# Performance work log

Hardware: AMD Instinct MI355X
Metric: run time of the kernel (lower is better)

The kernel has to match this reference:

```python
import jax, jax.numpy as jnp
import numpy as np

N_NODES = 100001      # total_nodes + 1
N_EDGES = 6400000     # avg degree ~64
LATENT_DIM = 32
N_LAYERS = 2


def setup_inputs() -> dict:
    key = jax.random.key(0)
    k1, k2, k3, k4 = jax.random.split(key, 4)
    emb_weight = jax.random.normal(k1, (N_NODES, LATENT_DIM), dtype=jnp.float32) * 0.1
    adj_vals = jax.random.uniform(k2, (N_EDGES,), dtype=jnp.float32)
    adj_row = jax.random.randint(k3, (N_EDGES,), 0, N_NODES, dtype=jnp.int32)
    adj_col = jax.random.randint(k4, (N_EDGES,), 0, N_NODES, dtype=jnp.int32)
    return {"emb_weight": emb_weight, "adj_vals": adj_vals,
            "adj_row": adj_row, "adj_col": adj_col}


def reference(emb_weight, adj_vals, adj_row, adj_col):
    n = emb_weight.shape[0]

    def spmm(x):
        # y[r] = sum_{e: row[e]==r} vals[e] * x[col[e]]  (torch.sparse.mm COO)
        gathered = adj_vals[:, None] * x[adj_col]  # [E, D]
        return jax.ops.segment_sum(gathered, adj_row, num_segments=n)

    emb = emb_weight
    acc = emb                      # layer-0 embedding
    for _ in range(N_LAYERS):
        emb = spmm(emb)
        acc = acc + emb
    # mean over (n_layers + 1) stacked embeddings
    return acc / jnp.float32(N_LAYERS + 1)
```

## Files before the change

kernel.cpp:

```cpp
#include <hip/hip_runtime.h>


constexpr int D = 32;
constexpr int RPB_LOG = 8;
constexpr int RPB = 1 << RPB_LOG;
constexpr int MAXNB = 512;
constexpr int TILE = 4096;
constexpr int PT2 = 512;
constexpr int CAP = 9728;
constexpr float QSCALE = 32768.0f;
constexpr float QINV = 1.0f / 32768.0f;

__device__ __forceinline__ unsigned short f2bf(float f) {
    unsigned u = __float_as_uint(f);
    unsigned r = (u + 0x7FFFu + ((u >> 16) & 1u)) >> 16;
    return (unsigned short)r;
}
__device__ __forceinline__ float bf2f(unsigned short h) {
    return __uint_as_float((unsigned)h << 16);
}

__global__ void zero_f32(float* __restrict__ p, int n) {
    int i = blockIdx.x * blockDim.x + threadIdx.x;
    if (i < n) p[i] = 0.0f;
}
__global__ void cast_bf16(const float* __restrict__ in,
                          unsigned short* __restrict__ out, int n) {
    int i = blockIdx.x * blockDim.x + threadIdx.x;
    if (i < n) out[i] = f2bf(in[i]);
}

__global__ __launch_bounds__(256) void tile_hist(
    const int* __restrict__ row, int* __restrict__ tileCnt, int nE, int NB) {
    __shared__ int h[MAXNB];
    int tile = blockIdx.x;
    int base = tile * TILE;
    int n = min(TILE, nE - base);
    int t = threadIdx.x;
    for (int i = t; i < NB; i += 256) h[i] = 0;
    __syncthreads();
    for (int i = t; i < n; i += 256)
        atomicAdd(&h[row[base + i] >> RPB_LOG], 1);
    __syncthreads();
    for (int i = t; i < NB; i += 256)
        tileCnt[(size_t)tile * NB + i] = h[i];
}

__global__ __launch_bounds__(256) void colscan(
    int* __restrict__ tileCnt, int* __restrict__ cnt, int nTiles, int NB) {
    __shared__ int s2[256];
    __shared__ int carryS;
    int b = blockIdx.x, t = threadIdx.x;
    if (t == 0) carryS = 0;
    __syncthreads();
    for (int c0 = 0; c0 < nTiles; c0 += 1024) {
        int v[4], idx[4];
        int sum = 0;
#pragma unroll
        for (int k = 0; k < 4; ++k) {
            idx[k] = c0 + t * 4 + k;
            v[k] = (idx[k] < nTiles) ? tileCnt[(size_t)idx[k] * NB + b] : 0;
            sum += v[k];
        }
        s2[t] = sum;
        __syncthreads();
        for (int o = 1; o < 256; o <<= 1) {
            int x = (t >= o) ? s2[t - o] : 0;
            __syncthreads();
            s2[t] += x;
            __syncthreads();
        }
        int run = ((t == 0) ? 0 : s2[t - 1]) + carryS;
#pragma unroll
        for (int k = 0; k < 4; ++k) {
            if (idx[k] < nTiles) tileCnt[(size_t)idx[k] * NB + b] = run;
            run += v[k];
        }
        __syncthreads();
        if (t == 0) carryS += s2[255];
        __syncthreads();
    }
    if (t == 0) cnt[b] = carryS;
}

__global__ __launch_bounds__(512) void scan_buckets(
    const int* __restrict__ cnt, int* __restrict__ bases, int NB, int nE) {
    __shared__ int s[MAXNB];
    int t = threadIdx.x;
    s[t] = (t < NB) ? cnt[t] : 0;
    __syncthreads();
    for (int o = 1; o < 512; o <<= 1) {
        int v = (t >= o) ? s[t - o] : 0;
        __syncthreads();
        s[t] += v;
        __syncthreads();
    }
    if (t < NB) bases[t] = (t == 0) ? 0 : s[t - 1];
    if (t == 0) bases[NB] = nE;
}

__global__ __launch_bounds__(PT2) void partition_edges2(
    const int* __restrict__ row, const int* __restrict__ col,
    const float* __restrict__ vals, const int* __restrict__ bases,
    const int* __restrict__ tileCnt, uint2* __restrict__ cv, int nE, int NB) {
    __shared__ uint2 buf[TILE];
    __shared__ unsigned short bkt[TILE];
    __shared__ int hist[MAXNB];
    __shared__ int runoff[MAXNB];
    __shared__ int s2[PT2];
    int t = threadIdx.x;
    int tile = blockIdx.x;
    int base = tile * TILE;
    int n = min(TILE, nE - base);
    if (n <= 0) return;
    for (int i = t; i < NB; i += PT2) hist[i] = 0;
    __syncthreads();
    for (int i = t; i < n; i += PT2)
        atomicAdd(&hist[row[base + i] >> RPB_LOG], 1);
    __syncthreads();
    {
        int a0 = (t < NB) ? hist[t] : 0;
        s2[t] = a0;
        __syncthreads();
        for (int o = 1; o < PT2; o <<= 1) {
            int v = (t >= o) ? s2[t - o] : 0;
            __syncthreads();
            s2[t] += v;
            __syncthreads();
        }
        if (t < NB) runoff[t] = s2[t] - a0;
    }
    __syncthreads();
    for (int i = t; i < NB; i += PT2)
        hist[i] = bases[i] + tileCnt[(size_t)tile * NB + i] - runoff[i];
    __syncthreads();
    for (int i = t; i < n; i += PT2) {
        int r = row[base + i];
        int b = r >> RPB_LOG;
        int slot = atomicAdd(&runoff[b], 1);
        float v = vals[base + i];
        int q = __float2int_rn(v * QSCALE);
        q = max(0, min(32767, q));
        uint2 p;
        p.x = (unsigned)col[base + i] | ((unsigned)(r & (RPB - 1)) << 17);
        p.y = (unsigned)q;
        buf[slot] = p;
        bkt[slot] = (unsigned short)b;
    }
    __syncthreads();
    for (int i = t; i < n; i += PT2)
        cv[hist[bkt[i]] + i] = buf[i];
}

__global__ __launch_bounds__(512) void csr_sort4(
    const int* __restrict__ bases, const uint2* __restrict__ cv,
    unsigned* __restrict__ cv2, int* __restrict__ rowptr, int n, int nE) {
    __shared__ unsigned stage[CAP];
    __shared__ int hist_s[RPB];
    __shared__ int cur_s[RPB];
    int t = threadIdx.x;
    int b = blockIdx.x >> 1;
    int h = blockIdx.x & 1;
    int s = bases[b], e = bases[b + 1];
    if (t < RPB) hist_s[t] = 0;
    __syncthreads();
    for (int i = s + t; i < e; i += 512)
        atomicAdd(&hist_s[cv[i].x >> 17], 1);
    __syncthreads();
    if (t < RPB) cur_s[t] = hist_s[t];
    __syncthreads();
    for (int o = 1; o < RPB; o <<= 1) {
        int v = 0;
        if (t < RPB && t >= o) v = cur_s[t - o];
        __syncthreads();
        if (t < RPB) cur_s[t] += v;
        __syncthreads();
    }
    int excl = 0;
    if (t < RPB) excl = (t == 0) ? 0 : cur_s[t - 1];
    int half_lo = h << 7;
    __syncthreads();
    int base_h = (half_lo == 0) ? 0 : cur_s[half_lo - 1];
    int end_h  = cur_s[half_lo + 127];
    int cnt_h  = end_h - base_h;
    __syncthreads();
    if (t < RPB) {
        if ((t >> 7) == h) {
            int r = (b << RPB_LOG) + t;
            if (r < n) rowptr[r] = s + excl;
            cur_s[t] = excl - base_h;
        }
    }
    if (b == 0 && h == 0 && t == 0) rowptr[n] = nE;
    __syncthreads();
    bool fits = (cnt_h <= CAP);
    for (int i = s + t; i < e; i += 512) {
        uint2 p = cv[i];
        int r = (int)(p.x >> 17);
        if ((r >> 7) != h) continue;
        int slot = atomicAdd(&cur_s[r], 1);
        unsigned packed = (p.x & 0x1FFFFu) | (p.y << 17);
        if (fits) stage[slot] = packed;
        else      cv2[s + base_h + slot] = packed;
    }
    __syncthreads();
    if (fits) {
        int dst = s + base_h;
        for (int j = t; j < cnt_h; j += 512)
            cv2[dst + j] = stage[j];
    }
}

__global__ __launch_bounds__(256) void spmm_l1(
    const int* __restrict__ ptr, const unsigned* __restrict__ cv,
    const unsigned short* __restrict__ xh, unsigned short* __restrict__ yh,
    int nRows) {
    int g = (blockIdx.x * 256 + threadIdx.x) >> 5;
    if (g >= nRows) return;
    int lane = threadIdx.x & 31;
    int e = ptr[g], end = ptr[g + 1];
    float acc = 0.0f;
    for (; e + 8 <= end; e += 8) {
        unsigned q0 = cv[e], q1 = cv[e + 1], q2 = cv[e + 2], q3 = cv[e + 3];
        unsigned q4 = cv[e + 4], q5 = cv[e + 5], q6 = cv[e + 6], q7 = cv[e + 7];
        float x0 = bf2f(xh[(size_t)(q0 & 0x1FFFFu) * D + lane]);
        float x1 = bf2f(xh[(size_t)(q1 & 0x1FFFFu) * D + lane]);
        float x2 = bf2f(xh[(size_t)(q2 & 0x1FFFFu) * D + lane]);
        float x3 = bf2f(xh[(size_t)(q3 & 0x1FFFFu) * D + lane]);
        float x4 = bf2f(xh[(size_t)(q4 & 0x1FFFFu) * D + lane]);
        float x5 = bf2f(xh[(size_t)(q5 & 0x1FFFFu) * D + lane]);
        float x6 = bf2f(xh[(size_t)(q6 & 0x1FFFFu) * D + lane]);
        float x7 = bf2f(xh[(size_t)(q7 & 0x1FFFFu) * D + lane]);
        acc += (float)(q0 >> 17) * x0;
        acc += (float)(q1 >> 17) * x1;
        acc += (float)(q2 >> 17) * x2;
        acc += (float)(q3 >> 17) * x3;
        acc += (float)(q4 >> 17) * x4;
        acc += (float)(q5 >> 17) * x5;
        acc += (float)(q6 >> 17) * x6;
        acc += (float)(q7 >> 17) * x7;
    }
    for (; e < end; ++e) {
        unsigned q = cv[e];
        acc += (float)(q >> 17) * bf2f(xh[(size_t)(q & 0x1FFFFu) * D + lane]);
    }
    yh[(size_t)g * D + lane] = f2bf(acc * QINV);
}

__global__ __launch_bounds__(256) void spmm_combine(
    const int* __restrict__ ptr, const unsigned* __restrict__ cv,
    const unsigned short* __restrict__ y1h, const float* __restrict__ emb,
    float* __restrict__ out, int nRows) {
    int g = (blockIdx.x * 256 + threadIdx.x) >> 5;
    if (g >= nRows) return;
    int lane = threadIdx.x & 31;
    int e = ptr[g], end = ptr[g + 1];
    float acc = 0.0f;
    for (; e + 8 <= end; e += 8) {
        unsigned q0 = cv[e], q1 = cv[e + 1], q2 = cv[e + 2], q3 = cv[e + 3];
        unsigned q4 = cv[e + 4], q5 = cv[e + 5], q6 = cv[e + 6], q7 = cv[e + 7];
        float x0 = bf2f(y1h[(size_t)(q0 & 0x1FFFFu) * D + lane]);
        float x1 = bf2f(y1h[(size_t)(q1 & 0x1FFFFu) * D + lane]);
        float x2 = bf2f(y1h[(size_t)(q2 & 0x1FFFFu) * D + lane]);
        float x3 = bf2f(y1h[(size_t)(q3 & 0x1FFFFu) * D + lane]);
        float x4 = bf2f(y1h[(size_t)(q4 & 0x1FFFFu) * D + lane]);
        float x5 = bf2f(y1h[(size_t)(q5 & 0x1FFFFu) * D + lane]);
        float x6 = bf2f(y1h[(size_t)(q6 & 0x1FFFFu) * D + lane]);
        float x7 = bf2f(y1h[(size_t)(q7 & 0x1FFFFu) * D + lane]);
        acc += (float)(q0 >> 17) * x0;
        acc += (float)(q1 >> 17) * x1;
        acc += (float)(q2 >> 17) * x2;
        acc += (float)(q3 >> 17) * x3;
        acc += (float)(q4 >> 17) * x4;
        acc += (float)(q5 >> 17) * x5;
        acc += (float)(q6 >> 17) * x6;
        acc += (float)(q7 >> 17) * x7;
    }
    for (; e < end; ++e) {
        unsigned q = cv[e];
        acc += (float)(q >> 17) * bf2f(y1h[(size_t)(q & 0x1FFFFu) * D + lane]);
    }
    size_t idx = (size_t)g * D + lane;
    out[idx] = (emb[idx] + bf2f(y1h[idx]) + acc * QINV) * (1.0f / 3.0f);
}

__global__ __launch_bounds__(256) void spmm_atomic(
    const int* __restrict__ row, const int* __restrict__ col,
    const float* __restrict__ vals, const float* __restrict__ x,
    float* __restrict__ y, int nEdges, float scale) {
    long long t = (long long)blockIdx.x * blockDim.x + threadIdx.x;
    int e = (int)(t >> 5);
    if (e >= nEdges) return;
    int d = (int)(t & 31);
    float g = vals[e] * scale * x[(long long)col[e] * D + d];
    atomicAdd(&y[(long long)row[e] * D + d], g);
}
__global__ void combine_third(const float* __restrict__ emb,
                              const float* __restrict__ y1,
                              float* __restrict__ out, int n) {
    int i = blockIdx.x * blockDim.x + threadIdx.x;
    if (i < n) out[i] = (emb[i] + y1[i]) * (1.0f / 3.0f);
}

extern "C" void kernel_launch(void* const* d_in, const int* in_sizes, int n_in,
                              void* d_out, int out_size, void* d_ws, size_t ws_size,
                              hipStream_t stream) {
    const float* emb  = (const float*)d_in[0];
    const float* vals = (const float*)d_in[1];
    const int*   row  = (const int*)d_in[2];
    const int*   col  = (const int*)d_in[3];
    float* out = (float*)d_out;

    const int nElem  = in_sizes[0];
    const int nEdges = in_sizes[1];
    const int n      = nElem / D;
    const int NB     = (n + RPB - 1) >> RPB_LOG;
    const int BLK = 256;
    const int nTiles = (nEdges + TILE - 1) / TILE;

    size_t off_cnt    = 0;
    size_t off_bases  = off_cnt + (size_t)NB * 4;
    size_t off_rowptr = off_bases + (size_t)(NB + 1) * 4;
    size_t off_cv     = (off_rowptr + (size_t)(n + 1) * 4 + 63) & ~(size_t)63;
    size_t off_cv2    = off_cv + (size_t)nEdges * 8;
    size_t need       = off_cv2 + (size_t)nEdges * 4;

    bool aliasFit   = ((size_t)nElem * 4 <= (size_t)nEdges * 8);
    bool tileCntFit = ((size_t)nTiles * NB * 4 <= (size_t)nEdges * 4);
    bool ok = (NB <= MAXNB) && (n <= 131072) && (ws_size >= need) &&
              aliasFit && tileCntFit;

    if (!ok) {
        if (ws_size < (size_t)nElem * 4) return;
        float* y1 = (float*)d_ws;
        zero_f32<<<(nElem + BLK - 1) / BLK, BLK, 0, stream>>>(y1, nElem);
        long long threads = (long long)nEdges * 32;
        int blocks = (int)((threads + BLK - 1) / BLK);
        spmm_atomic<<<blocks, BLK, 0, stream>>>(row, col, vals, emb, y1, nEdges, 1.0f);
        combine_third<<<(nElem + BLK - 1) / BLK, BLK, 0, stream>>>(emb, y1, out, nElem);
        spmm_atomic<<<blocks, BLK, 0, stream>>>(row, col, vals, y1, out, nEdges, 1.0f / 3.0f);
        return;
    }

    char* ws = (char*)d_ws;
    int*            cnt     = (int*)(ws + off_cnt);
    int*            bases   = (int*)(ws + off_bases);
    int*            rowptr  = (int*)(ws + off_rowptr);
    uint2*          cv      = (uint2*)(ws + off_cv);
    unsigned*       cv2     = (unsigned*)(ws + off_cv2);
    int*            tileCnt = (int*)(ws + off_cv2);
    unsigned short* y1h     = (unsigned short*)(ws + off_cv);
    unsigned short* embh    = (unsigned short*)(ws + off_cv + (size_t)nElem * 2);

    tile_hist<<<nTiles, 256, 0, stream>>>(row, tileCnt, nEdges, NB);

    colscan<<<NB, 256, 0, stream>>>(tileCnt, cnt, nTiles, NB);

    scan_buckets<<<1, 512, 0, stream>>>(cnt, bases, NB, nEdges);

    partition_edges2<<<nTiles, PT2, 0, stream>>>(row, col, vals, bases,
                                                 tileCnt, cv, nEdges, NB);

    csr_sort4<<<2 * NB, 512, 0, stream>>>(bases, cv, cv2, rowptr, n, nEdges);

    cast_bf16<<<(nElem + BLK - 1) / BLK, BLK, 0, stream>>>(emb, embh, nElem);

    int rowBlocks = (n * 32 + BLK - 1) / BLK;
    spmm_l1<<<rowBlocks, BLK, 0, stream>>>(rowptr, cv2, embh, y1h, n);

    spmm_combine<<<rowBlocks, BLK, 0, stream>>>(rowptr, cv2, y1h, emb, out, n);
}
```

Baseline: 272.4 us.

## Quantize gathered embeddings to int8 with per-tensor absmax scale for both SpMM layers

Replaces the bf16 gathered feature tensors with int8 copies scaled by a per-tensor absmax. This needs an absmax reduction kernel, an extra quantize pass after layer 1, and a fused max reduction inside the layer-1 SpMM. Both SpMM loops now accumulate in integers, which halves the bytes per random gather row and is meant to cut memory traffic. In exchange it adds launches and loses accuracy: int8 with a single global scale is coarse and may push the output past the tolerance.

```diff
diff --git a/kernel.cpp b/kernel.cpp
--- a/kernel.cpp
+++ b/kernel.cpp
@@ -24,10 +24,46 @@
     int i = blockIdx.x * blockDim.x + threadIdx.x;
     if (i < n) p[i] = 0.0f;
 }
-__global__ void cast_bf16(const float* __restrict__ in,
-                          unsigned short* __restrict__ out, int n) {
+__global__ void zero2_u32(unsigned* __restrict__ p) {
+    p[0] = 0u;
+    p[1] = 0u;
+}
+
+__global__ __launch_bounds__(256) void absmax_f32(
+    const float* __restrict__ in, unsigned* __restrict__ outBits, int n) {
+    __shared__ float s[4];
+    float m = 0.0f;
+    for (int i = blockIdx.x * 256 + threadIdx.x; i < n; i += gridDim.x * 256)
+        m = fmaxf(m, fabsf(in[i]));
+    for (int o = 32; o > 0; o >>= 1) m = fmaxf(m, __shfl_down(m, o, 64));
+    int wid = threadIdx.x >> 6;
+    if ((threadIdx.x & 63) == 0) s[wid] = m;
+    __syncthreads();
+    if (threadIdx.x == 0) {
+        float mm = fmaxf(fmaxf(s[0], s[1]), fmaxf(s[2], s[3]));
+        atomicMax(outBits, __float_as_uint(mm));
+    }
+}
+
+__global__ void quant8_f32(const float* __restrict__ in,
+                           const unsigned* __restrict__ maxBits,
+                           signed char* __restrict__ out, int n) {
     int i = blockIdx.x * blockDim.x + threadIdx.x;
-    if (i < n) out[i] = f2bf(in[i]);
+    if (i >= n) return;
+    float mx = fmaxf(__uint_as_float(*maxBits), 1e-20f);
+    float inv = 127.0f / mx;
+    int q = __float2int_rn(in[i] * inv);
+    out[i] = (signed char)max(-127, min(127, q));
+}
+__global__ void quant8_bf16(const unsigned short* __restrict__ in,
+                            const unsigned* __restrict__ maxBits,
+                            signed char* __restrict__ out, int n) {
+    int i = blockIdx.x * blockDim.x + threadIdx.x;
+    if (i >= n) return;
+    float mx = fmaxf(__uint_as_float(*maxBits), 1e-20f);
+    float inv = 127.0f / mx;
+    int q = __float2int_rn(bf2f(in[i]) * inv);
+    out[i] = (signed char)max(-127, min(127, q));
 }
 
 __global__ __launch_bounds__(256) void tile_hist(
@@ -211,77 +247,95 @@
     }
 }
 
-__global__ __launch_bounds__(256) void spmm_l1(
+__global__ __launch_bounds__(256) void spmm_l1_q8(
     const int* __restrict__ ptr, const unsigned* __restrict__ cv,
-    const unsigned short* __restrict__ xh, unsigned short* __restrict__ yh,
+    const signed char* __restrict__ xq, const unsigned* __restrict__ xMaxBits,
+    unsigned short* __restrict__ yh, unsigned* __restrict__ yMaxBits,
     int nRows) {
+    __shared__ float smax[4];
     int g = (blockIdx.x * 256 + threadIdx.x) >> 5;
-    if (g >= nRows) return;
     int lane = threadIdx.x & 31;
-    int e = ptr[g], end = ptr[g + 1];
-    float acc = 0.0f;
-    for (; e + 8 <= end; e += 8) {
-        unsigned q0 = cv[e], q1 = cv[e + 1], q2 = cv[e + 2], q3 = cv[e + 3];
-        unsigned q4 = cv[e + 4], q5 = cv[e + 5], q6 = cv[e + 6], q7 = cv[e + 7];
-        float x0 = bf2f(xh[(size_t)(q0 & 0x1FFFFu) * D + lane]);
-        float x1 = bf2f(xh[(size_t)(q1 & 0x1FFFFu) * D + lane]);
-        float x2 = bf2f(xh[(size_t)(q2 & 0x1FFFFu) * D + lane]);
-        float x3 = bf2f(xh[(size_t)(q3 & 0x1FFFFu) * D + lane]);
-        float x4 = bf2f(xh[(size_t)(q4 & 0x1FFFFu) * D + lane]);
-        float x5 = bf2f(xh[(size_t)(q5 & 0x1FFFFu) * D + lane]);
-        float x6 = bf2f(xh[(size_t)(q6 & 0x1FFFFu) * D + lane]);
-        float x7 = bf2f(xh[(size_t)(q7 & 0x1FFFFu) * D + lane]);
-        acc += (float)(q0 >> 17) * x0;
-        acc += (float)(q1 >> 17) * x1;
-        acc += (float)(q2 >> 17) * x2;
-        acc += (float)(q3 >> 17) * x3;
-        acc += (float)(q4 >> 17) * x4;
-        acc += (float)(q5 >> 17) * x5;
-        acc += (float)(q6 >> 17) * x6;
-        acc += (float)(q7 >> 17) * x7;
-    }
-    for (; e < end; ++e) {
-        unsigned q = cv[e];
-        acc += (float)(q >> 17) * bf2f(xh[(size_t)(q & 0x1FFFFu) * D + lane]);
-    }
-    yh[(size_t)g * D + lane] = f2bf(acc * QINV);
-}
-
-__global__ __launch_bounds__(256) void spmm_combine(
+    float av = 0.0f;
+    if (g < nRows) {
+        int e = ptr[g], end = ptr[g + 1];
+        int acc = 0;
+        for (; e + 8 <= end; e += 8) {
+            unsigned q0 = cv[e], q1 = cv[e + 1], q2 = cv[e + 2], q3 = cv[e + 3];
+            unsigned q4 = cv[e + 4], q5 = cv[e + 5], q6 = cv[e + 6], q7 = cv[e + 7];
+            int x0 = xq[(size_t)(q0 & 0x1FFFFu) * D + lane];
+            int x1 = xq[(size_t)(q1 & 0x1FFFFu) * D + lane];
+            int x2 = xq[(size_t)(q2 & 0x1FFFFu) * D + lane];
+            int x3 = xq[(size_t)(q3 & 0x1FFFFu) * D + lane];
+            int x4 = xq[(size_t)(q4 & 0x1FFFFu) * D + lane];
+            int x5 = xq[(size_t)(q5 & 0x1FFFFu) * D + lane];
+            int x6 = xq[(size_t)(q6 & 0x1FFFFu) * D + lane];
+            int x7 = xq[(size_t)(q7 & 0x1FFFFu) * D + lane];
+            acc += (int)(q0 >> 17) * x0;
+            acc += (int)(q1 >> 17) * x1;
+            acc += (int)(q2 >> 17) * x2;
+            acc += (int)(q3 >> 17) * x3;
+            acc += (int)(q4 >> 17) * x4;
+            acc += (int)(q5 >> 17) * x5;
+            acc += (int)(q6 >> 17) * x6;
+            acc += (int)(q7 >> 17) * x7;
+        }
+        for (; e < end; ++e) {
+            unsigned q = cv[e];
+            acc += (int)(q >> 17) * (int)xq[(size_t)(q & 0x1FFFFu) * D + lane];
+        }
+        float xs = fmaxf(__uint_as_float(*xMaxBits), 1e-20f) * (1.0f / 127.0f);
+        float y = (float)acc * (QINV * xs);
+        yh[(size_t)g * D + lane] = f2bf(y);
+        av = fabsf(y);
+    }
+    for (int o = 32; o > 0; o >>= 1) av = fmaxf(av, __shfl_down(av, o, 64));
+    int wid = threadIdx.x >> 6;
+    if ((threadIdx.x & 63) == 0) smax[wid] = av;
+    __syncthreads();
+    if (threadIdx.x == 0) {
+        float mm = fmaxf(fmaxf(smax[0], smax[1]), fmaxf(smax[2], smax[3]));
+        atomicMax(yMaxBits, __float_as_uint(mm));
+    }
+}
+
+__global__ __launch_bounds__(256) void spmm_combine_q8(
     const int* __restrict__ ptr, const unsigned* __restrict__ cv,
+    const signed char* __restrict__ y1q, const unsigned* __restrict__ yMaxBits,
     const unsigned short* __restrict__ y1h, const float* __restrict__ emb,
     float* __restrict__ out, int nRows) {
     int g = (blockIdx.x * 256 + threadIdx.x) >> 5;
     if (g >= nRows) return;
     int lane = threadIdx.x & 31;
     int e = ptr[g], end = ptr[g + 1];
-    float acc = 0.0f;
+    int acc = 0;
     for (; e + 8 <= end; e += 8) {
         unsigned q0 = cv[e], q1 = cv[e + 1], q2 = cv[e + 2], q3 = cv[e + 3];
         unsigned q4 = cv[e + 4], q5 = cv[e + 5], q6 = cv[e + 6], q7 = cv[e + 7];
-        float x0 = bf2f(y1h[(size_t)(q0 & 0x1FFFFu) * D + lane]);
-        float x1 = bf2f(y1h[(size_t)(q1 & 0x1FFFFu) * D + lane]);
-        float x2 = bf2f(y1h[(size_t)(q2 & 0x1FFFFu) * D + lane]);
-        float x3 = bf2f(y1h[(size_t)(q3 & 0x1FFFFu) * D + lane]);
-        float x4 = bf2f(y1h[(size_t)(q4 & 0x1FFFFu) * D + lane]);
-        float x5 = bf2f(y1h[(size_t)(q5 & 0x1FFFFu) * D + lane]);
-        float x6 = bf2f(y1h[(size_t)(q6 & 0x1FFFFu) * D + lane]);
-        float x7 = bf2f(y1h[(size_t)(q7 & 0x1FFFFu) * D + lane]);
-        acc += (float)(q0 >> 17) * x0;
-        acc += (float)(q1 >> 17) * x1;
-        acc += (float)(q2 >> 17) * x2;
-        acc += (float)(q3 >> 17) * x3;
-        acc += (float)(q4 >> 17) * x4;
-        acc += (float)(q5 >> 17) * x5;
-        acc += (float)(q6 >> 17) * x6;
-        acc += (float)(q7 >> 17) * x7;
+        int x0 = y1q[(size_t)(q0 & 0x1FFFFu) * D + lane];
+        int x1 = y1q[(size_t)(q1 & 0x1FFFFu) * D + lane];
+        int x2 = y1q[(size_t)(q2 & 0x1FFFFu) * D + lane];
+        int x3 = y1q[(size_t)(q3 & 0x1FFFFu) * D + lane];
+        int x4 = y1q[(size_t)(q4 & 0x1FFFFu) * D + lane];
+        int x5 = y1q[(size_t)(q5 & 0x1FFFFu) * D + lane];
+        int x6 = y1q[(size_t)(q6 & 0x1FFFFu) * D + lane];
+        int x7 = y1q[(size_t)(q7 & 0x1FFFFu) * D + lane];
+        acc += (int)(q0 >> 17) * x0;
+        acc += (int)(q1 >> 17) * x1;
+        acc += (int)(q2 >> 17) * x2;
+        acc += (int)(q3 >> 17) * x3;
+        acc += (int)(q4 >> 17) * x4;
+        acc += (int)(q5 >> 17) * x5;
+        acc += (int)(q6 >> 17) * x6;
+        acc += (int)(q7 >> 17) * x7;
     }
     for (; e < end; ++e) {
         unsigned q = cv[e];
-        acc += (float)(q >> 17) * bf2f(y1h[(size_t)(q & 0x1FFFFu) * D + lane]);
-    }
+        acc += (int)(q >> 17) * (int)y1q[(size_t)(q & 0x1FFFFu) * D + lane];
+    }
+    float ys = fmaxf(__uint_as_float(*yMaxBits), 1e-20f) * (1.0f / 127.0f);
     size_t idx = (size_t)g * D + lane;
-    out[idx] = (emb[idx] + bf2f(y1h[idx]) + acc * QINV) * (1.0f / 3.0f);
+    out[idx] = (emb[idx] + bf2f(y1h[idx]) + (float)acc * (QINV * ys))
+               * (1.0f / 3.0f);
 }
 
 __global__ __launch_bounds__(256) void spmm_atomic(
@@ -321,7 +375,8 @@
     size_t off_cnt    = 0;
     size_t off_bases  = off_cnt + (size_t)NB * 4;
     size_t off_rowptr = off_bases + (size_t)(NB + 1) * 4;
-    size_t off_cv     = (off_rowptr + (size_t)(n + 1) * 4 + 63) & ~(size_t)63;
+    size_t off_scal   = off_rowptr + (size_t)(n + 1) * 4;
+    size_t off_cv     = (off_scal + 8 + 63) & ~(size_t)63;
     size_t off_cv2    = off_cv + (size_t)nEdges * 8;
     size_t need       = off_cv2 + (size_t)nEdges * 4;
 
@@ -346,11 +401,16 @@
     int*            cnt     = (int*)(ws + off_cnt);
     int*            bases   = (int*)(ws + off_bases);
     int*            rowptr  = (int*)(ws + off_rowptr);
+    unsigned*       scal    = (unsigned*)(ws + off_scal);
     uint2*          cv      = (uint2*)(ws + off_cv);
     unsigned*       cv2     = (unsigned*)(ws + off_cv2);
     int*            tileCnt = (int*)(ws + off_cv2);
     unsigned short* y1h     = (unsigned short*)(ws + off_cv);
-    unsigned short* embh    = (unsigned short*)(ws + off_cv + (size_t)nElem * 2);
+    signed char*    xq      = (signed char*)(ws + off_cv + (size_t)nElem * 2);
+    signed char*    y1q     = (signed char*)(ws + off_cv + (size_t)nElem * 3);
+
+    zero2_u32<<<1, 1, 0, stream>>>(scal);
+    absmax_f32<<<1024, 256, 0, stream>>>(emb, &scal[0], nElem);
 
     tile_hist<<<nTiles, 256, 0, stream>>>(row, tileCnt, nEdges, NB);
 
@@ -363,10 +423,14 @@
 
     csr_sort4<<<2 * NB, 512, 0, stream>>>(bases, cv, cv2, rowptr, n, nEdges);
 
-    cast_bf16<<<(nElem + BLK - 1) / BLK, BLK, 0, stream>>>(emb, embh, nElem);
+    quant8_f32<<<(nElem + BLK - 1) / BLK, BLK, 0, stream>>>(emb, &scal[0], xq, nElem);
 
     int rowBlocks = (n * 32 + BLK - 1) / BLK;
-    spmm_l1<<<rowBlocks, BLK, 0, stream>>>(rowptr, cv2, embh, y1h, n);
-
-    spmm_combine<<<rowBlocks, BLK, 0, stream>>>(rowptr, cv2, y1h, emb, out, n);
-}
+    spmm_l1_q8<<<rowBlocks, BLK, 0, stream>>>(rowptr, cv2, xq, &scal[0],
+                                              y1h, &scal[1], n);
+
+    quant8_bf16<<<(nElem + BLK - 1) / BLK, BLK, 0, stream>>>(y1h, &scal[1], y1q, nElem);
+
+    spmm_combine_q8<<<rowBlocks, BLK, 0, stream>>>(rowptr, cv2, y1q, &scal[1],
+                                                   y1h, emb, out, n);
+}
```

Result: slower. 363.2 us (+33.3%).
